# Kernel tuning notes

Measured on AMD Instinct MI355X. Metric: run time of the kernel, lower is better.

## Reference

```python
import jax, jax.numpy as jnp
import numpy as np

N_NODES = 100000
N_EDGES = 3200000
DIMS = [1, 64, 32, 16, 1]  # GCNConv channel sizes from __init__


def _add_self_loops(edge_index, n):
    loop = jnp.arange(n, dtype=edge_index.dtype)
    src = jnp.concatenate([edge_index[0], loop])
    dst = jnp.concatenate([edge_index[1], loop])
    return src, dst


def _deg_inv_sqrt(dst, n):
    # symmetric GCN norm: deg over destination nodes of A + I (edge_weight = 1)
    deg = jax.ops.segment_sum(jnp.ones_like(dst, dtype=jnp.float32), dst, num_segments=n)
    return jnp.where(deg > 0, jax.lax.rsqrt(deg), 0.0)


def _gcn_conv(x, src, dst, dinv, W, b, n):
    h = x @ W                                   # [N, out] transform first (PyG order)
    coef = dinv[src] * dinv[dst]                # [E+N] edge normalization
    out = jax.ops.segment_sum(coef[:, None] * h[src], dst, num_segments=n)
    return out + b


def setup_inputs() -> dict:
    key = jax.random.key(0)
    ks = jax.random.split(key, 12)
    x = jax.random.normal(ks[0], (N_NODES, DIMS[0]), dtype=jnp.float32)
    edge_index = jax.random.randint(ks[1], (2, N_EDGES), 0, N_NODES, dtype=jnp.int64)
    params = {}
    for i in range(4):
        fin, fout = DIMS[i], DIMS[i + 1]
        scale = 1.0 / np.sqrt(fin)
        params[f"W{i+1}"] = jax.random.uniform(ks[2 + 2 * i], (fin, fout), jnp.float32, -scale, scale)
        params[f"b{i+1}"] = jnp.zeros((fout,), jnp.float32)
    return {"x": x, "edge_index": edge_index, **params}


def reference(x, edge_index, W1, b1, W2, b2, W3, b3, W4, b4):
    n = x.shape[0]
    src, dst = _add_self_loops(edge_index, n)
    dinv = _deg_inv_sqrt(dst, n)
    h = jax.nn.relu(_gcn_conv(x, src, dst, dinv, W1, b1, n))
    h = jax.nn.relu(_gcn_conv(h, src, dst, dinv, W2, b2, n))
    h = jax.nn.relu(_gcn_conv(h, src, dst, dinv, W3, b3, n))
    h = _gcn_conv(h, src, dst, dinv, W4, b4, n)
    return h
```

## Files before the change

### kernel.cpp

```cpp
#include <hip/hip_runtime.h>

#define NPB_SHIFT 8
#define NPB 256
#define EPB 4096
#define EPT 16
#define MAXB 512
#define BCAP 9216
#define SRC_BITS 17
#define SRC_MASK 0x1FFFFu

__global__ __launch_bounds__(256) void partition_kernel(const int* __restrict__ src,
                                                        const int* __restrict__ dst,
                                                        unsigned int* __restrict__ bcur,
                                                        unsigned int* __restrict__ staged, int E, int NB) {
    __shared__ unsigned int hist[MAXB], sc[MAXB], lbase[MAXB], gbase[MAXB];
    __shared__ unsigned int stage[EPB];
    __shared__ unsigned short sbuck[EPB];
    int start = blockIdx.x * EPB;
    int cnt = min(EPB, E - start);
    for (int j = threadIdx.x; j < MAXB; j += 256) hist[j] = 0u;
    __syncthreads();

    unsigned int rec[EPT], rnk[EPT], bkt[EPT];
#pragma unroll
    for (int u = 0; u < EPT; ++u) {
        int k = u * 256 + threadIdx.x;
        if (k < cnt) {
            unsigned int d = (unsigned int)dst[start + k];
            unsigned int s = (unsigned int)src[start + k];
            unsigned int b = d >> NPB_SHIFT;
            rec[u] = ((d & (NPB - 1)) << SRC_BITS) | s;
            bkt[u] = b;
            rnk[u] = atomicAdd(&hist[b], 1u);
        }
    }
    __syncthreads();
    {
        int i0 = threadIdx.x, i1 = threadIdx.x + 256;
        sc[i0] = hist[i0]; sc[i1] = hist[i1];
        __syncthreads();
        for (int o = 1; o < MAXB; o <<= 1) {
            unsigned int v0 = (i0 >= o) ? sc[i0 - o] : 0u;
            unsigned int v1 = (i1 >= o) ? sc[i1 - o] : 0u;
            __syncthreads();
            sc[i0] += v0; sc[i1] += v1;
            __syncthreads();
        }
    }
    for (int j = threadIdx.x; j < MAXB; j += 256) {
        unsigned int c = hist[j];
        lbase[j] = sc[j] - c;
        gbase[j] = (j < NB && c) ? atomicAdd(&bcur[j], c) : 0u;
    }
    __syncthreads();
#pragma unroll
    for (int u = 0; u < EPT; ++u) {
        int k = u * 256 + threadIdx.x;
        if (k < cnt) {
            unsigned int pos = lbase[bkt[u]] + rnk[u];
            stage[pos] = rec[u];
            sbuck[pos] = (unsigned short)bkt[u];
        }
    }
    __syncthreads();
    for (int t = threadIdx.x; t < cnt; t += 256) {
        unsigned int b = sbuck[t];
        staged[(size_t)gbase[b] + (t - lbase[b])] = stage[t];
    }
}

__global__ __launch_bounds__(256) void build_csr_kernel(const unsigned int* __restrict__ staged,
                                                        const unsigned int* __restrict__ bcur,
                                                        const float* __restrict__ x,
                                                        unsigned int* __restrict__ csr,
                                                        unsigned int* __restrict__ off,
                                                        unsigned int* __restrict__ deg,
                                                        float* __restrict__ dinv,
                                                        float* __restrict__ ttx, int N) {
    __shared__ unsigned int cnt[NPB], loff[NPB], ncur[NPB];
    int b = blockIdx.x;
    unsigned int base = (unsigned int)b * BCAP;
    unsigned int m = bcur[b] - base;
    int node0 = b << NPB_SHIFT;
    cnt[threadIdx.x] = 0u;
    __syncthreads();
    for (unsigned int t = threadIdx.x; t < m; t += 256)
        atomicAdd(&cnt[staged[(size_t)base + t] >> SRC_BITS], 1u);
    __syncthreads();
    unsigned int v = cnt[threadIdx.x];
    loff[threadIdx.x] = v;
    __syncthreads();
    for (int o = 1; o < NPB; o <<= 1) {
        unsigned int a = (threadIdx.x >= (unsigned)o) ? loff[threadIdx.x - o] : 0u;
        __syncthreads();
        loff[threadIdx.x] += a;
        __syncthreads();
    }
    unsigned int ex = loff[threadIdx.x] - v;
    ncur[threadIdx.x] = ex;
    int node = node0 + threadIdx.x;
    if (node < N) {
        off[node] = base + ex;
        deg[node] = v;
        float di = 1.0f / sqrtf((float)(v + 1u));
        dinv[node] = di;
        ttx[node] = di * x[node];
    }
    __syncthreads();
    for (unsigned int t = threadIdx.x; t < m; t += 256) {
        unsigned int rec = staged[(size_t)base + t];
        unsigned int p = atomicAdd(&ncur[rec >> SRC_BITS], 1u);
        csr[(size_t)base + p] = rec & SRC_MASK;
    }
}

__global__ __launch_bounds__(256) void lut_kernel(const float* __restrict__ W1, const float* __restrict__ b1,
                                                  const float* __restrict__ W2,
                                                  float* __restrict__ Alut, float* __restrict__ Blut,
                                                  float* __restrict__ tvals,
                                                  unsigned int* __restrict__ bcur, int NB) {
    __shared__ float w1[64], bb[64], tv[64];
    __shared__ int rnk[64];
    __shared__ float sW2[64 * 32];
    __shared__ double red[2][256];
    int tid = threadIdx.x;
    if (blockIdx.x == 0) {
        for (int t = tid; t < NB; t += 256) bcur[t] = (unsigned int)t * BCAP;
    }
    if (tid < 64) {
        float w = W1[tid], b = b1[tid];
        w1[tid] = w; bb[tid] = b;
        tv[tid] = (w != 0.f) ? (-b / w) : __uint_as_float(0x7F800000u);
    }
    for (int t = tid; t < 64 * 32; t += 256) sW2[t] = W2[t];
    __syncthreads();
    if (tid < 64) {
        int r = 0;
        float tj = tv[tid];
        for (int k = 0; k < 64; ++k)
            if (w1[k] != 0.f && (tv[k] < tj || (tv[k] == tj && k < tid))) ++r;
        rnk[tid] = r;
        if (blockIdx.x == 0) tvals[tid] = tv[tid];
    }
    __syncthreads();
    int s = blockIdx.x;
    int c = tid & 31, slice = tid >> 5;
    double da = 0.0, db = 0.0;
#pragma unroll
    for (int u = 0; u < 8; ++u) {
        int j = slice * 8 + u;
        float w = w1[j];
        bool act = (w > 0.f) ? (rnk[j] < s) : ((w < 0.f) ? (rnk[j] >= s) : (bb[j] > 0.f));
        if (act) {
            double w2 = (double)sW2[j * 32 + c];
            da += (double)w * w2;
            db += (double)bb[j] * w2;
        }
    }
    red[0][tid] = da; red[1][tid] = db;
    __syncthreads();
    for (int o = 128; o >= 32; o >>= 1) {
        if (tid < o) { red[0][tid] += red[0][tid + o]; red[1][tid] += red[1][tid + o]; }
        __syncthreads();
    }
    if (tid < 32) {
        Alut[s * 32 + tid] = (float)red[0][tid];
        Blut[s * 32 + tid] = (float)red[1][tid];
    }
}

__global__ __launch_bounds__(256) void gather1_kernel(const unsigned int* __restrict__ csr,
                                                      const unsigned int* __restrict__ off,
                                                      const unsigned int* __restrict__ deg,
                                                      const float* __restrict__ dinv,
                                                      const float* __restrict__ tt,
                                                      const float* __restrict__ tvals,
                                                      uint4* __restrict__ recs, int N) {
    __shared__ float st[64];
    for (int t = threadIdx.x; t < 64; t += 256) st[t] = tvals[t];
    __syncthreads();
    int tid = blockIdx.x * 256 + threadIdx.x;
    int i = tid >> 2, l = tid & 3;
    if (i >= N) return;
    unsigned int o = off[i], n = deg[i];
    float acc0 = 0.f, acc1 = 0.f;
    unsigned int k = l;
    for (; k + 4 < n; k += 8) { acc0 += tt[csr[o + k]]; acc1 += tt[csr[o + k + 4]]; }
    if (k < n) acc0 += tt[csr[o + k]];
    float acc = acc0 + acc1;
    acc += __shfl_xor(acc, 1, 4);
    acc += __shfl_xor(acc, 2, 4);
    float di = dinv[i];
    float a = di * (acc + tt[i]);
    unsigned int cv = 0;
#pragma unroll
    for (int j = 0; j < 16; ++j) cv += (st[l * 16 + j] < a) ? 1u : 0u;
    cv += __shfl_xor(cv, 1, 4);
    cv += __shfl_xor(cv, 2, 4);
    if (l == 0) recs[i] = make_uint4(__float_as_uint(a * di), __float_as_uint(di), cv, 0u);
}

#define G2_ITERS 4
#define FMA4(R, ACC)                                                          \
    {                                                                         \
        float4 A_ = sA2[(R).z * 8 + cc], B_ = sB2[(R).z * 8 + cc];            \
        float p_ = __uint_as_float((R).x), q_ = __uint_as_float((R).y);       \
        (ACC).x = fmaf(A_.x, p_, fmaf(B_.x, q_, (ACC).x));                    \
        (ACC).y = fmaf(A_.y, p_, fmaf(B_.y, q_, (ACC).y));                    \
        (ACC).z = fmaf(A_.z, p_, fmaf(B_.z, q_, (ACC).z));                    \
        (ACC).w = fmaf(A_.w, p_, fmaf(B_.w, q_, (ACC).w));                    \
    }
__global__ __launch_bounds__(256) void gather2t3_kernel(const unsigned int* __restrict__ csr,
                                                        const unsigned int* __restrict__ off,
                                                        const unsigned int* __restrict__ deg,
                                                        const float* __restrict__ dinv,
                                                        const uint4* __restrict__ recs,
                                                        const float* __restrict__ Alut, const float* __restrict__ Blut,
                                                        const float* __restrict__ b2, const float* __restrict__ W3,
                                                        float* __restrict__ tt3, int N) {
    __shared__ float4 sA2[65 * 8], sB2[65 * 8];
    __shared__ float2 sW3p[32 * 8];
    __shared__ float sb2[32];
    for (int t = threadIdx.x; t < 65 * 8; t += 256) {
        int s = t >> 3, q = t & 7;
        sA2[t] = make_float4(Alut[s * 32 + q], Alut[s * 32 + q + 8],
                             Alut[s * 32 + q + 16], Alut[s * 32 + q + 24]);
        sB2[t] = make_float4(Blut[s * 32 + q], Blut[s * 32 + q + 8],
                             Blut[s * 32 + q + 16], Blut[s * 32 + q + 24]);
    }
    for (int t = threadIdx.x; t < 32 * 8; t += 256) {
        int k = t >> 3, q = t & 7;
        sW3p[t] = make_float2(W3[k * 16 + q], W3[k * 16 + q + 8]);
    }
    if (threadIdx.x < 32) sb2[threadIdx.x] = b2[threadIdx.x];
    __syncthreads();

    int g = threadIdx.x >> 3, cc = threadIdx.x & 7;
    for (int iter = 0; iter < G2_ITERS; ++iter) {
        int d = blockIdx.x * (32 * G2_ITERS) + iter * 32 + g;
        if (d >= N) continue;
        float dd = dinv[d];
        unsigned int o = off[d], n = deg[d];
        uint4 rs = recs[d];
        float ps = __uint_as_float(rs.x), qs = __uint_as_float(rs.y);
        float4 As = sA2[rs.z * 8 + cc], Bs = sB2[rs.z * 8 + cc];
        float4 aP, aQ;
        aP.x = fmaf(As.x, ps, Bs.x * qs); aP.y = fmaf(As.y, ps, Bs.y * qs);
        aP.z = fmaf(As.z, ps, Bs.z * qs); aP.w = fmaf(As.w, ps, Bs.w * qs);
        aQ = make_float4(0.f, 0.f, 0.f, 0.f);
        unsigned int P = n >> 1;
        if (P >= 2) {
            unsigned int c0 = csr[o], c1 = csr[o + 1];
            unsigned int c2 = csr[o + 2], c3 = csr[o + 3];
            uint4 r0 = recs[c0], r1 = recs[c1];
            for (unsigned int j = 0; j + 2 < P; ++j) {
                unsigned int base = o + 2 * j;
                unsigned int nc0 = csr[base + 4], nc1 = csr[base + 5];
                uint4 nr0 = recs[c2], nr1 = recs[c3];
                FMA4(r0, aP); FMA4(r1, aQ);
                r0 = nr0; r1 = nr1; c2 = nc0; c3 = nc1;
            }
            uint4 m0 = recs[c2], m1 = recs[c3];
            FMA4(r0, aP); FMA4(r1, aQ);
            FMA4(m0, aP); FMA4(m1, aQ);
        } else if (P == 1) {
            uint4 r0 = recs[csr[o]], r1 = recs[csr[o + 1]];
            FMA4(r0, aP); FMA4(r1, aQ);
        }
        if (n & 1u) {
            uint4 r0 = recs[csr[o + n - 1]];
            FMA4(r0, aP);
        }
        float hv0 = fmaxf(fmaf(dd, aP.x + aQ.x, sb2[cc]), 0.f);
        float hv1 = fmaxf(fmaf(dd, aP.y + aQ.y, sb2[cc + 8]), 0.f);
        float hv2 = fmaxf(fmaf(dd, aP.z + aQ.z, sb2[cc + 16]), 0.f);
        float hv3 = fmaxf(fmaf(dd, aP.w + aQ.w, sb2[cc + 24]), 0.f);

        float t0 = 0.f, t1 = 0.f;
#pragma unroll
        for (int l2 = 0; l2 < 8; ++l2) {
            float hk = __shfl(hv0, l2, 8);
            float2 w = sW3p[l2 * 8 + cc];
            t0 = fmaf(hk, w.x, t0); t1 = fmaf(hk, w.y, t1);
        }
#pragma unroll
        for (int l2 = 0; l2 < 8; ++l2) {
            float hk = __shfl(hv1, l2, 8);
            float2 w = sW3p[(8 + l2) * 8 + cc];
            t0 = fmaf(hk, w.x, t0); t1 = fmaf(hk, w.y, t1);
        }
#pragma unroll
        for (int l2 = 0; l2 < 8; ++l2) {
            float hk = __shfl(hv2, l2, 8);
            float2 w = sW3p[(16 + l2) * 8 + cc];
            t0 = fmaf(hk, w.x, t0); t1 = fmaf(hk, w.y, t1);
        }
#pragma unroll
        for (int l2 = 0; l2 < 8; ++l2) {
            float hk = __shfl(hv3, l2, 8);
            float2 w = sW3p[(24 + l2) * 8 + cc];
            t0 = fmaf(hk, w.x, t0); t1 = fmaf(hk, w.y, t1);
        }
        tt3[(size_t)d * 16 + cc] = dd * t0;
        tt3[(size_t)d * 16 + cc + 8] = dd * t1;
    }
}

__global__ __launch_bounds__(256) void gather3t4_kernel(const unsigned int* __restrict__ csr,
                                                        const unsigned int* __restrict__ off,
                                                        const unsigned int* __restrict__ deg,
                                                        const float* __restrict__ dinv,
                                                        const float* __restrict__ tt3,
                                                        const float* __restrict__ b3, const float* __restrict__ W4,
                                                        float* __restrict__ tt4, int N) {
    int tid = blockIdx.x * 256 + threadIdx.x;
    int d = tid >> 2, l = tid & 3;
    if (d >= N) return;
    float dd = dinv[d];
    unsigned int o = off[d], n = deg[d];
    const float4* t34 = reinterpret_cast<const float4*>(tt3);
    float4 acc = t34[(size_t)d * 4 + l];
    float4 acc1 = make_float4(0.f, 0.f, 0.f, 0.f);
    unsigned int k = 0;
    if (n >= 4) {
        unsigned int s0 = csr[o], s1 = csr[o + 1], s2 = csr[o + 2], s3 = csr[o + 3];
        k = 4;
        for (; k + 3 < n; k += 4) {
            unsigned int t0 = csr[o + k], t1 = csr[o + k + 1], t2 = csr[o + k + 2], t3 = csr[o + k + 3];
            float4 v0 = t34[(size_t)s0 * 4 + l];
            float4 v1 = t34[(size_t)s1 * 4 + l];
            float4 v2 = t34[(size_t)s2 * 4 + l];
            float4 v3 = t34[(size_t)s3 * 4 + l];
            acc.x += v0.x + v2.x; acc.y += v0.y + v2.y; acc.z += v0.z + v2.z; acc.w += v0.w + v2.w;
            acc1.x += v1.x + v3.x; acc1.y += v1.y + v3.y; acc1.z += v1.z + v3.z; acc1.w += v1.w + v3.w;
            s0 = t0; s1 = t1; s2 = t2; s3 = t3;
        }
        {
            float4 v0 = t34[(size_t)s0 * 4 + l];
            float4 v1 = t34[(size_t)s1 * 4 + l];
            float4 v2 = t34[(size_t)s2 * 4 + l];
            float4 v3 = t34[(size_t)s3 * 4 + l];
            acc.x += v0.x + v2.x; acc.y += v0.y + v2.y; acc.z += v0.z + v2.z; acc.w += v0.w + v2.w;
            acc1.x += v1.x + v3.x; acc1.y += v1.y + v3.y; acc1.z += v1.z + v3.z; acc1.w += v1.w + v3.w;
        }
    }
    for (; k < n; ++k) {
        float4 v0 = t34[(size_t)csr[o + k] * 4 + l];
        acc.x += v0.x; acc.y += v0.y; acc.z += v0.z; acc.w += v0.w;
    }
    acc.x += acc1.x; acc.y += acc1.y; acc.z += acc1.z; acc.w += acc1.w;
    float4 b3v = reinterpret_cast<const float4*>(b3)[l];
    float4 w4v = reinterpret_cast<const float4*>(W4)[l];
    float v = fmaxf(fmaf(dd, acc.x, b3v.x), 0.f) * w4v.x;
    v = fmaf(fmaxf(fmaf(dd, acc.y, b3v.y), 0.f), w4v.y, v);
    v = fmaf(fmaxf(fmaf(dd, acc.z, b3v.z), 0.f), w4v.z, v);
    v = fmaf(fmaxf(fmaf(dd, acc.w, b3v.w), 0.f), w4v.w, v);
    v += __shfl_xor(v, 1, 4);
    v += __shfl_xor(v, 2, 4);
    if (l == 0) tt4[d] = dd * v;
}

__global__ void gather4_kernel(const unsigned int* __restrict__ csr, const unsigned int* __restrict__ off,
                               const unsigned int* __restrict__ deg, const float* __restrict__ dinv,
                               const float* __restrict__ tt, const float* __restrict__ b4,
                               float* __restrict__ out, int N) {
    int tid = blockIdx.x * blockDim.x + threadIdx.x;
    int i = tid >> 2, l = tid & 3;
    if (i >= N) return;
    unsigned int o = off[i], n = deg[i];
    float acc0 = 0.f, acc1 = 0.f;
    unsigned int k = l;
    for (; k + 4 < n; k += 8) { acc0 += tt[csr[o + k]]; acc1 += tt[csr[o + k + 4]]; }
    if (k < n) acc0 += tt[csr[o + k]];
    float acc = acc0 + acc1;
    acc += __shfl_xor(acc, 1, 4);
    acc += __shfl_xor(acc, 2, 4);
    if (l == 0) out[i] = dinv[i] * (acc + tt[i]) + b4[0];
}

extern "C" void kernel_launch(void* const* d_in, const int* in_sizes, int n_in,
                              void* d_out, int out_size, void* d_ws, size_t ws_size,
                              hipStream_t stream) {
    const float* x  = (const float*)d_in[0];
    const int* eidx = (const int*)d_in[1];
    const float* W1 = (const float*)d_in[2];
    const float* b1 = (const float*)d_in[3];
    const float* W2 = (const float*)d_in[4];
    const float* b2 = (const float*)d_in[5];
    const float* W3 = (const float*)d_in[6];
    const float* b3 = (const float*)d_in[7];
    const float* W4 = (const float*)d_in[8];
    const float* b4 = (const float*)d_in[9];
    float* out = (float*)d_out;

    const int N = in_sizes[0];
    const int E = in_sizes[1] / 2;
    const int* src = eidx;
    const int* dst = eidx + E;
    const int NB = (N + NPB - 1) >> NPB_SHIFT;

    char* ws = (char*)d_ws;
    unsigned int* bcur  = (unsigned int*)ws;  ws += MAXB * 4;
    float* tvals = (float*)ws;                ws += 64 * 4;
    float* Alut  = (float*)ws;                ws += 65 * 32 * 4;
    float* Blut  = (float*)ws;                ws += 65 * 32 * 4;
    unsigned int* off = (unsigned int*)ws;    ws += (size_t)N * 4;
    unsigned int* deg = (unsigned int*)ws;    ws += (size_t)N * 4;
    float* dinv = (float*)ws;                 ws += (size_t)N * 4;
    float* ttx  = (float*)ws;                 ws += (size_t)N * 4;
    float* tt4  = (float*)ws;                 ws += (size_t)N * 4;
    uint4* recs = (uint4*)ws;                 ws += (size_t)N * 16;
    unsigned int* csr = (unsigned int*)ws;    ws += (size_t)NB * BCAP * 4;
    unsigned int* staged = (unsigned int*)ws;
    float* tt3 = (float*)staged;

    const int nPartBlocks = (E + EPB - 1) / EPB;

    lut_kernel<<<65, 256, 0, stream>>>(W1, b1, W2, Alut, Blut, tvals, bcur, NB);
    partition_kernel<<<nPartBlocks, 256, 0, stream>>>(src, dst, bcur, staged, E, NB);
    build_csr_kernel<<<NB, 256, 0, stream>>>(staged, bcur, x, csr, off, deg, dinv, ttx, N);

    gather1_kernel<<<((size_t)N * 4 + 255) / 256, 256, 0, stream>>>(csr, off, deg, dinv, ttx, tvals, recs, N);
    gather2t3_kernel<<<(N + 32 * G2_ITERS - 1) / (32 * G2_ITERS), 256, 0, stream>>>(csr, off, deg, dinv, recs, Alut, Blut, b2, W3, tt3, N);
    gather3t4_kernel<<<((size_t)N * 4 + 255) / 256, 256, 0, stream>>>(csr, off, deg, dinv, tt3, b3, W4, tt4, N);
    gather4_kernel<<<((size_t)N * 4 + 255) / 256, 256, 0, stream>>>(csr, off, deg, dinv, tt4, b4, out, N);
}
```

Baseline: 188.8 us.

## Split layer-3 gather into two feature-half passes with a partial buffer

The 16-wide layer-3 gather is split into two kernel launches, each gathering 8 features (two float4 lanes per node) over the full edge list. The first pass writes a partial layer-4 dot product to a new buffer and the second adds it and scales. The aim is to halve the gathered working set per pass so the source table fits better in cache. The cost is reading the CSR indices twice and an extra launch.

```diff
diff --git a/kernel.cpp b/kernel.cpp
--- a/kernel.cpp
+++ b/kernel.cpp
@@ -306,58 +306,59 @@
     }
 }
 
-__global__ __launch_bounds__(256) void gather3t4_kernel(const unsigned int* __restrict__ csr,
-                                                        const unsigned int* __restrict__ off,
-                                                        const unsigned int* __restrict__ deg,
-                                                        const float* __restrict__ dinv,
-                                                        const float* __restrict__ tt3,
-                                                        const float* __restrict__ b3, const float* __restrict__ W4,
-                                                        float* __restrict__ tt4, int N) {
+template<int HALF>
+__global__ __launch_bounds__(256) void gather3t4_half_kernel(const unsigned int* __restrict__ csr,
+                                                             const unsigned int* __restrict__ off,
+                                                             const unsigned int* __restrict__ deg,
+                                                             const float* __restrict__ dinv,
+                                                             const float* __restrict__ tt3,
+                                                             const float* __restrict__ b3, const float* __restrict__ W4,
+                                                             float* __restrict__ partial,
+                                                             float* __restrict__ tt4, int N) {
     int tid = blockIdx.x * 256 + threadIdx.x;
-    int d = tid >> 2, l = tid & 3;
+    int d = tid >> 1, l = tid & 1;
     if (d >= N) return;
     float dd = dinv[d];
     unsigned int o = off[d], n = deg[d];
     const float4* t34 = reinterpret_cast<const float4*>(tt3);
-    float4 acc = t34[(size_t)d * 4 + l];
+    const int fi = 2 * HALF + l;
+    float4 acc = t34[(size_t)d * 4 + fi];
     float4 acc1 = make_float4(0.f, 0.f, 0.f, 0.f);
     unsigned int k = 0;
-    if (n >= 4) {
-        unsigned int s0 = csr[o], s1 = csr[o + 1], s2 = csr[o + 2], s3 = csr[o + 3];
-        k = 4;
-        for (; k + 3 < n; k += 4) {
-            unsigned int t0 = csr[o + k], t1 = csr[o + k + 1], t2 = csr[o + k + 2], t3 = csr[o + k + 3];
-            float4 v0 = t34[(size_t)s0 * 4 + l];
-            float4 v1 = t34[(size_t)s1 * 4 + l];
-            float4 v2 = t34[(size_t)s2 * 4 + l];
-            float4 v3 = t34[(size_t)s3 * 4 + l];
-            acc.x += v0.x + v2.x; acc.y += v0.y + v2.y; acc.z += v0.z + v2.z; acc.w += v0.w + v2.w;
-            acc1.x += v1.x + v3.x; acc1.y += v1.y + v3.y; acc1.z += v1.z + v3.z; acc1.w += v1.w + v3.w;
-            s0 = t0; s1 = t1; s2 = t2; s3 = t3;
+    if (n >= 2) {
+        unsigned int s0 = csr[o], s1 = csr[o + 1];
+        k = 2;
+        for (; k + 1 < n; k += 2) {
+            unsigned int t0 = csr[o + k], t1 = csr[o + k + 1];
+            float4 v0 = t34[(size_t)s0 * 4 + fi];
+            float4 v1 = t34[(size_t)s1 * 4 + fi];
+            acc.x += v0.x; acc.y += v0.y; acc.z += v0.z; acc.w += v0.w;
+            acc1.x += v1.x; acc1.y += v1.y; acc1.z += v1.z; acc1.w += v1.w;
+            s0 = t0; s1 = t1;
         }
         {
-            float4 v0 = t34[(size_t)s0 * 4 + l];
-            float4 v1 = t34[(size_t)s1 * 4 + l];
-            float4 v2 = t34[(size_t)s2 * 4 + l];
-            float4 v3 = t34[(size_t)s3 * 4 + l];
-            acc.x += v0.x + v2.x; acc.y += v0.y + v2.y; acc.z += v0.z + v2.z; acc.w += v0.w + v2.w;
-            acc1.x += v1.x + v3.x; acc1.y += v1.y + v3.y; acc1.z += v1.z + v3.z; acc1.w += v1.w + v3.w;
-        }
-    }
-    for (; k < n; ++k) {
-        float4 v0 = t34[(size_t)csr[o + k] * 4 + l];
+            float4 v0 = t34[(size_t)s0 * 4 + fi];
+            float4 v1 = t34[(size_t)s1 * 4 + fi];
+            acc.x += v0.x; acc.y += v0.y; acc.z += v0.z; acc.w += v0.w;
+            acc1.x += v1.x; acc1.y += v1.y; acc1.z += v1.z; acc1.w += v1.w;
+        }
+    }
+    if (k < n) {
+        float4 v0 = t34[(size_t)csr[o + k] * 4 + fi];
         acc.x += v0.x; acc.y += v0.y; acc.z += v0.z; acc.w += v0.w;
     }
     acc.x += acc1.x; acc.y += acc1.y; acc.z += acc1.z; acc.w += acc1.w;
-    float4 b3v = reinterpret_cast<const float4*>(b3)[l];
-    float4 w4v = reinterpret_cast<const float4*>(W4)[l];
+    float4 b3v = reinterpret_cast<const float4*>(b3)[fi];
+    float4 w4v = reinterpret_cast<const float4*>(W4)[fi];
     float v = fmaxf(fmaf(dd, acc.x, b3v.x), 0.f) * w4v.x;
     v = fmaf(fmaxf(fmaf(dd, acc.y, b3v.y), 0.f), w4v.y, v);
     v = fmaf(fmaxf(fmaf(dd, acc.z, b3v.z), 0.f), w4v.z, v);
     v = fmaf(fmaxf(fmaf(dd, acc.w, b3v.w), 0.f), w4v.w, v);
-    v += __shfl_xor(v, 1, 4);
-    v += __shfl_xor(v, 2, 4);
-    if (l == 0) tt4[d] = dd * v;
+    v += __shfl_xor(v, 1, 2);
+    if (l == 0) {
+        if (HALF == 0) partial[d] = v;
+        else           tt4[d] = dd * (partial[d] + v);
+    }
 }
 
 __global__ void gather4_kernel(const unsigned int* __restrict__ csr, const unsigned int* __restrict__ off,
@@ -409,6 +410,7 @@
     float* dinv = (float*)ws;                 ws += (size_t)N * 4;
     float* ttx  = (float*)ws;                 ws += (size_t)N * 4;
     float* tt4  = (float*)ws;                 ws += (size_t)N * 4;
+    float* part = (float*)ws;                 ws += (size_t)N * 4;
     uint4* recs = (uint4*)ws;                 ws += (size_t)N * 16;
     unsigned int* csr = (unsigned int*)ws;    ws += (size_t)NB * BCAP * 4;
     unsigned int* staged = (unsigned int*)ws;
@@ -422,6 +424,7 @@
 
     gather1_kernel<<<((size_t)N * 4 + 255) / 256, 256, 0, stream>>>(csr, off, deg, dinv, ttx, tvals, recs, N);
     gather2t3_kernel<<<(N + 32 * G2_ITERS - 1) / (32 * G2_ITERS), 256, 0, stream>>>(csr, off, deg, dinv, recs, Alut, Blut, b2, W3, tt3, N);
-    gather3t4_kernel<<<((size_t)N * 4 + 255) / 256, 256, 0, stream>>>(csr, off, deg, dinv, tt3, b3, W4, tt4, N);
+    gather3t4_half_kernel<0><<<((size_t)N * 2 + 255) / 256, 256, 0, stream>>>(csr, off, deg, dinv, tt3, b3, W4, part, tt4, N);
+    gather3t4_half_kernel<1><<<((size_t)N * 2 + 255) / 256, 256, 0, stream>>>(csr, off, deg, dinv, tt3, b3, W4, part, tt4, N);
     gather4_kernel<<<((size_t)N * 4 + 255) / 256, 256, 0, stream>>>(csr, off, deg, dinv, tt4, b4, out, N);
 }
```

Result: slower. 243.3 us (+28.9%).
